# Kernel optimization log

Measured on AMD Instinct MI355X. Metric: run time of the kernel, lower is better.

Reference implementation:

```python
import jax, jax.numpy as jnp
import numpy as np

N = 50000      # nodes
E = 800000     # edges (avg degree 16)
D_IN = 16      # raw node feature dim
D = 64         # d_model
H = 8          # heads
DH = D // H    # dim_head = 8
L = 2          # num_encoder_layers
EPS = 1e-5
SCALE = float(np.sqrt(DH))


def _xavier(key, shape):
    fan_in, fan_out = shape[-2], shape[-1]
    a = float(np.sqrt(6.0 / (fan_in + fan_out)))
    return jax.random.uniform(key, shape, jnp.float32, -a, a)


def setup_inputs() -> dict:
    key = jax.random.key(0)
    ks = jax.random.split(key, 20)
    feat = jax.random.normal(ks[0], (N, D_IN), jnp.float32)
    src = jax.random.randint(ks[1], (E,), 0, N, jnp.int32)
    dst = jax.random.randint(ks[2], (E,), 0, N, jnp.int32)
    return {
        "feat": feat,
        "src": src,
        "dst": dst,
        "W_emb": _xavier(ks[3], (D_IN, D)),
        "b_emb": jnp.zeros((D,), jnp.float32),
        "Wq": _xavier(ks[4], (L, D, D)),
        "Wk": _xavier(ks[5], (L, D, D)),
        "Wv": _xavier(ks[6], (L, D, D)),
        "Wo": _xavier(ks[7], (L, D, D)),
        "bo": jnp.zeros((L, D), jnp.float32),
        "bn1_g": jnp.ones((L, D), jnp.float32),
        "bn1_b": jnp.zeros((L, D), jnp.float32),
        "W1": _xavier(ks[8], (L, D, 2 * D)),
        "b1": jnp.zeros((L, 2 * D), jnp.float32),
        "W2": _xavier(ks[9], (L, 2 * D, D)),
        "b2": jnp.zeros((L, D), jnp.float32),
        "bn2_g": jnp.ones((L, D), jnp.float32),
        "bn2_b": jnp.zeros((L, D), jnp.float32),
    }


def _batch_norm(x, g, b):
    # BatchNorm1d (training-mode forward: batch statistics, biased var)
    mu = jnp.mean(x, axis=0)
    var = jnp.var(x, axis=0)
    return (x - mu) / jnp.sqrt(var + EPS) * g + b


def _layer(h, src, dst, Wq, Wk, Wv, Wo, bo, bn1_g, bn1_b, W1, b1, W2, b2, bn2_g, bn2_b):
    h_in1 = h
    Q = (h @ Wq).reshape(N, H, DH)
    K = (h @ Wk).reshape(N, H, DH)
    V = (h @ Wv).reshape(N, H, DH)
    # SDDMM: per-edge dot(K[src], Q[dst]) -> [E, H]
    e = jnp.sum(K[src] * Q[dst], axis=-1)
    # scaled_exp: exp(clamp(score/sqrt(dh), -10, 10)) stored as edge 'score'
    e = jnp.exp(jnp.clip(e / SCALE, -10.0, 10.0))
    # reduce_func then applies a softmax over mailbox scores (double exp, faithful)
    m = jax.ops.segment_max(e, dst, num_segments=N)          # [N, H]
    w = jnp.exp(e - m[dst])                                   # [E, H]
    s = jax.ops.segment_sum(w, dst, num_segments=N)           # [N, H]
    alpha = w / s[dst]                                        # [E, H]
    out = jax.ops.segment_sum(alpha[:, :, None] * V[src], dst, num_segments=N)
    h = out.reshape(N, D) @ Wo + bo
    h = _batch_norm(h_in1 + h, bn1_g, bn1_b)
    h_in2 = h
    h = jax.nn.relu(h @ W1 + b1) @ W2 + b2
    h = _batch_norm(h + h_in2, bn2_g, bn2_b)
    return h


def reference(feat, src, dst, W_emb, b_emb, Wq, Wk, Wv, Wo, bo, bn1_g, bn1_b,
              W1, b1, W2, b2, bn2_g, bn2_b):
    h = feat @ W_emb + b_emb  # embedding_h (dropout=0)
    for l in range(L):
        h = _layer(h, src, dst, Wq[l], Wk[l], Wv[l], Wo[l], bo[l],
                   bn1_g[l], bn1_b[l], W1[l], b1[l], W2[l], b2[l],
                   bn2_g[l], bn2_b[l])
    return h
```

## Files before the change

kernel.cpp:

```cpp
#include <hip/hip_runtime.h>

#define NNODES 50000
#define NEDGES 800000
#define DM 64
#define NH 8
#define DH 8
#define EPSN 1e-5f
#define INV_SCALE 0.3535533905932738f
#define SCAN_BLOCKS 200
#define SCAN_CHUNK  250

template<int KA, int KB, int R, bool RELU, bool RES, bool STATS, bool BNRES>
__global__ __launch_bounds__(256, 4) void gemm_k(const float* __restrict__ A,
    const float* __restrict__ W, int woff,
    const float* __restrict__ bias, int boff,
    float* __restrict__ C, float* __restrict__ stats,
    const float* __restrict__ bnstats, const float* __restrict__ bng, int bgoff,
    const float* __restrict__ bnb, int bboff, int Nrows)
{
    constexpr int CG   = KB / 4;
    constexpr int RG   = 256 / CG;
    constexpr int ROWS = RG * R;
    constexpr int APAD = KA + 4;
    constexpr int KAq  = KA / 4;

    __shared__ __align__(16) float sW[KA * KB];
    __shared__ __align__(16) float sA[ROWS * APAD];

    const int tid  = threadIdx.x;
    const int row0 = blockIdx.x * ROWS;

    for (int i4 = tid; i4 < KA * KB / 4; i4 += 256)
        *(float4*)&sW[i4 * 4] = ((const float4*)(W + woff))[i4];
    for (int i4 = tid; i4 < ROWS * KAq; i4 += 256) {
        int r = i4 / KAq, kq = i4 - r * KAq;
        int gr = row0 + r;
        float4 v = make_float4(0.f, 0.f, 0.f, 0.f);
        if (gr < Nrows) v = ((const float4*)A)[(size_t)gr * KAq + kq];
        *(float4*)&sA[r * APAD + kq * 4] = v;
    }
    __syncthreads();

    const int cg = tid % CG, rg = tid / CG;
    const int c0 = cg * 4, r0 = rg * R;

    float4 acc[R];
#pragma unroll
    for (int rr = 0; rr < R; rr++) acc[rr] = make_float4(0.f, 0.f, 0.f, 0.f);

#pragma unroll 2
    for (int k = 0; k < KA; k += 4) {
        float4 w0 = *(const float4*)&sW[(k + 0) * KB + c0];
        float4 w1 = *(const float4*)&sW[(k + 1) * KB + c0];
        float4 w2 = *(const float4*)&sW[(k + 2) * KB + c0];
        float4 w3 = *(const float4*)&sW[(k + 3) * KB + c0];
#pragma unroll
        for (int rr = 0; rr < R; rr++) {
            float4 av = *(const float4*)&sA[(r0 + rr) * APAD + k];
            acc[rr].x += av.x * w0.x + av.y * w1.x + av.z * w2.x + av.w * w3.x;
            acc[rr].y += av.x * w0.y + av.y * w1.y + av.z * w2.y + av.w * w3.y;
            acc[rr].z += av.x * w0.z + av.y * w1.z + av.z * w2.z + av.w * w3.z;
            acc[rr].w += av.x * w0.w + av.y * w1.w + av.z * w2.w + av.w * w3.w;
        }
    }

    float4 bv = make_float4(0.f, 0.f, 0.f, 0.f);
    if (bias) {
        bv.x = bias[boff + c0];     bv.y = bias[boff + c0 + 1];
        bv.z = bias[boff + c0 + 2]; bv.w = bias[boff + c0 + 3];
    }

    float4 scR = make_float4(1.f, 1.f, 1.f, 1.f);
    float4 ofR = make_float4(0.f, 0.f, 0.f, 0.f);
    if (BNRES) {
        const float inv_n = 1.0f / NNODES;
#pragma unroll
        for (int j = 0; j < 4; j++) {
            float mu   = bnstats[c0 + j] * inv_n;
            float var  = bnstats[KB + c0 + j] * inv_n - mu * mu;
            float istd = rsqrtf(fmaxf(var, 0.f) + EPSN);
            float s    = istd * bng[bgoff + c0 + j];
            ((float*)&scR)[j] = s;
            ((float*)&ofR)[j] = bnb[bboff + c0 + j] - mu * s;
        }
    }

    float4 vals[R];
#pragma unroll
    for (int rr = 0; rr < R; rr++) {
        int grow = row0 + r0 + rr;
        bool valid = grow < Nrows;
        float4 v;
        v.x = acc[rr].x + bv.x; v.y = acc[rr].y + bv.y;
        v.z = acc[rr].z + bv.z; v.w = acc[rr].w + bv.w;
        if (RELU) {
            v.x = fmaxf(v.x, 0.f); v.y = fmaxf(v.y, 0.f);
            v.z = fmaxf(v.z, 0.f); v.w = fmaxf(v.w, 0.f);
        }
        if (valid) {
            if (RES) {
                float4 old = *(const float4*)&C[(size_t)grow * KB + c0];
                if (BNRES) {
                    old.x = old.x * scR.x + ofR.x;
                    old.y = old.y * scR.y + ofR.y;
                    old.z = old.z * scR.z + ofR.z;
                    old.w = old.w * scR.w + ofR.w;
                }
                v.x += old.x; v.y += old.y; v.z += old.z; v.w += old.w;
            }
            *(float4*)&C[(size_t)grow * KB + c0] = v;
        } else {
            v = make_float4(0.f, 0.f, 0.f, 0.f);
        }
        vals[rr] = v;
    }

    if (STATS) {
        __syncthreads();
        float4 cs = make_float4(0.f, 0.f, 0.f, 0.f);
#pragma unroll
        for (int rr = 0; rr < R; rr++) {
            cs.x += vals[rr].x; cs.y += vals[rr].y;
            cs.z += vals[rr].z; cs.w += vals[rr].w;
        }
        *(float4*)&sA[rg * KB + c0] = cs;
        __syncthreads();
        if (tid < KB) {
            float s = 0.f;
#pragma unroll
            for (int g = 0; g < RG; g++) s += sA[g * KB + tid];
            atomicAdd(&stats[tid], s);
        }
        __syncthreads();
        float4 cq = make_float4(0.f, 0.f, 0.f, 0.f);
#pragma unroll
        for (int rr = 0; rr < R; rr++) {
            cq.x += vals[rr].x * vals[rr].x; cq.y += vals[rr].y * vals[rr].y;
            cq.z += vals[rr].z * vals[rr].z; cq.w += vals[rr].w * vals[rr].w;
        }
        *(float4*)&sA[rg * KB + c0] = cq;
        __syncthreads();
        if (tid < KB) {
            float s = 0.f;
#pragma unroll
            for (int g = 0; g < RG; g++) s += sA[g * KB + tid];
            atomicAdd(&stats[KB + tid], s);
        }
    }
}

template<bool BNIN>
__global__ __launch_bounds__(256, 4) void qkv_k(const float* __restrict__ A,
    const float* __restrict__ Wq, const float* __restrict__ Wk,
    const float* __restrict__ Wv, int woff,
    float* __restrict__ Qo, float* __restrict__ Ko, float* __restrict__ Vo,
    const float* __restrict__ bnstats, const float* __restrict__ bng, int bgoff,
    const float* __restrict__ bnb, int bboff, int Nrows)
{
    constexpr int APAD = 68;
    __shared__ __align__(16) float sW[64 * 64];
    __shared__ __align__(16) float sA[64 * APAD];

    const int tid  = threadIdx.x;
    const int row0 = blockIdx.x * 64;

    {
        const int kq = tid & 15, cc = kq * 4;
        float4 sc = make_float4(1.f, 1.f, 1.f, 1.f);
        float4 of = make_float4(0.f, 0.f, 0.f, 0.f);
        if (BNIN) {
            const float inv_n = 1.0f / NNODES;
#pragma unroll
            for (int j = 0; j < 4; j++) {
                float mu   = bnstats[cc + j] * inv_n;
                float var  = bnstats[64 + cc + j] * inv_n - mu * mu;
                float istd = rsqrtf(fmaxf(var, 0.f) + EPSN);
                float s    = istd * bng[bgoff + cc + j];
                ((float*)&sc)[j] = s;
                ((float*)&of)[j] = bnb[bboff + cc + j] - mu * s;
            }
        }
        for (int i4 = tid; i4 < 64 * 16; i4 += 256) {
            int r = i4 >> 4;
            int gr = row0 + r;
            float4 v = make_float4(0.f, 0.f, 0.f, 0.f);
            if (gr < Nrows) {
                v = ((const float4*)A)[(size_t)gr * 16 + kq];
                if (BNIN) {
                    v.x = v.x * sc.x + of.x; v.y = v.y * sc.y + of.y;
                    v.z = v.z * sc.z + of.z; v.w = v.w * sc.w + of.w;
                }
            }
            *(float4*)&sA[r * APAD + cc] = v;
        }
    }

    const float* Ws[3]   = {Wq, Wk, Wv};
    float*       Outs[3] = {Qo, Ko, Vo};

    const int cg = tid & 15, rg = tid >> 4;
    const int c0 = cg * 4, r0 = rg * 4;

    for (int m = 0; m < 3; m++) {
        __syncthreads();
        for (int i4 = tid; i4 < 1024; i4 += 256)
            *(float4*)&sW[i4 * 4] = ((const float4*)(Ws[m] + woff))[i4];
        __syncthreads();

        float4 acc[4];
#pragma unroll
        for (int rr = 0; rr < 4; rr++) acc[rr] = make_float4(0.f, 0.f, 0.f, 0.f);

#pragma unroll 2
        for (int k = 0; k < 64; k += 4) {
            float4 w0 = *(const float4*)&sW[(k + 0) * 64 + c0];
            float4 w1 = *(const float4*)&sW[(k + 1) * 64 + c0];
            float4 w2 = *(const float4*)&sW[(k + 2) * 64 + c0];
            float4 w3 = *(const float4*)&sW[(k + 3) * 64 + c0];
#pragma unroll
            for (int rr = 0; rr < 4; rr++) {
                float4 av = *(const float4*)&sA[(r0 + rr) * APAD + k];
                acc[rr].x += av.x * w0.x + av.y * w1.x + av.z * w2.x + av.w * w3.x;
                acc[rr].y += av.x * w0.y + av.y * w1.y + av.z * w2.y + av.w * w3.y;
                acc[rr].z += av.x * w0.z + av.y * w1.z + av.z * w2.z + av.w * w3.z;
                acc[rr].w += av.x * w0.w + av.y * w1.w + av.z * w2.w + av.w * w3.w;
            }
        }

#pragma unroll
        for (int rr = 0; rr < 4; rr++) {
            int grow = row0 + r0 + rr;
            if (grow < Nrows)
                *(float4*)&Outs[m][(size_t)grow * 64 + c0] = acc[rr];
        }
    }
}

__global__ __launch_bounds__(256, 2) void ffn_k(float* __restrict__ H,
    const float* __restrict__ W1, int w1off,
    const float* __restrict__ b1, int b1off,
    const float* __restrict__ W2, int w2off,
    const float* __restrict__ b2, int b2off,
    const float* __restrict__ bnstats,
    const float* __restrict__ bng, int bgoff,
    const float* __restrict__ bnb, int bboff,
    float* __restrict__ stats2, int Nrows)
{
    constexpr int APAD = 68, FPAD = 132;
    __shared__ __align__(16) float sW[128 * 64];
    __shared__ __align__(16) float sA[32 * APAD];
    __shared__ __align__(16) float sF[32 * FPAD];

    const int tid  = threadIdx.x;
    const int row0 = blockIdx.x * 32;

    for (int i4 = tid; i4 < 2048; i4 += 256)
        *(float4*)&sW[i4 * 4] = ((const float4*)(W1 + w1off))[i4];

    {
        const int kq = tid & 15, cc = kq * 4;
        const float inv_n = 1.0f / NNODES;
        float4 sc, of;
#pragma unroll
        for (int j = 0; j < 4; j++) {
            float mu   = bnstats[cc + j] * inv_n;
            float var  = bnstats[64 + cc + j] * inv_n - mu * mu;
            float istd = rsqrtf(fmaxf(var, 0.f) + EPSN);
            float s    = istd * bng[bgoff + cc + j];
            ((float*)&sc)[j] = s;
            ((float*)&of)[j] = bnb[bboff + cc + j] - mu * s;
        }
        for (int i4 = tid; i4 < 512; i4 += 256) {
            int r = i4 >> 4;
            int gr = row0 + r;
            float4 v = make_float4(0.f, 0.f, 0.f, 0.f);
            if (gr < Nrows) {
                v = ((const float4*)H)[(size_t)gr * 16 + kq];
                v.x = v.x * sc.x + of.x; v.y = v.y * sc.y + of.y;
                v.z = v.z * sc.z + of.z; v.w = v.w * sc.w + of.w;
            }
            *(float4*)&sA[r * APAD + cc] = v;
        }
    }
    __syncthreads();

    {
        const int cg = tid & 31, rg = tid >> 5;
        const int c0 = cg * 4, r0 = rg * 4;
        float4 acc[4];
#pragma unroll
        for (int rr = 0; rr < 4; rr++) acc[rr] = make_float4(0.f, 0.f, 0.f, 0.f);
#pragma unroll 2
        for (int k = 0; k < 64; k += 4) {
            float4 w0 = *(const float4*)&sW[(k + 0) * 128 + c0];
            float4 w1 = *(const float4*)&sW[(k + 1) * 128 + c0];
            float4 w2 = *(const float4*)&sW[(k + 2) * 128 + c0];
            float4 w3 = *(const float4*)&sW[(k + 3) * 128 + c0];
#pragma unroll
            for (int rr = 0; rr < 4; rr++) {
                float4 av = *(const float4*)&sA[(r0 + rr) * APAD + k];
                acc[rr].x += av.x * w0.x + av.y * w1.x + av.z * w2.x + av.w * w3.x;
                acc[rr].y += av.x * w0.y + av.y * w1.y + av.z * w2.y + av.w * w3.y;
                acc[rr].z += av.x * w0.z + av.y * w1.z + av.z * w2.z + av.w * w3.z;
                acc[rr].w += av.x * w0.w + av.y * w1.w + av.z * w2.w + av.w * w3.w;
            }
        }
        float4 bb;
        bb.x = b1[b1off + c0];     bb.y = b1[b1off + c0 + 1];
        bb.z = b1[b1off + c0 + 2]; bb.w = b1[b1off + c0 + 3];
#pragma unroll
        for (int rr = 0; rr < 4; rr++) {
            float4 v;
            v.x = fmaxf(acc[rr].x + bb.x, 0.f);
            v.y = fmaxf(acc[rr].y + bb.y, 0.f);
            v.z = fmaxf(acc[rr].z + bb.z, 0.f);
            v.w = fmaxf(acc[rr].w + bb.w, 0.f);
            *(float4*)&sF[(r0 + rr) * FPAD + c0] = v;
        }
    }
    __syncthreads();

    for (int i4 = tid; i4 < 2048; i4 += 256)
        *(float4*)&sW[i4 * 4] = ((const float4*)(W2 + w2off))[i4];
    __syncthreads();

    const int cg = tid & 15, rg = tid >> 4;
    const int c0 = cg * 4, r0 = rg * 2;
    float4 acc[2];
#pragma unroll
    for (int rr = 0; rr < 2; rr++) acc[rr] = make_float4(0.f, 0.f, 0.f, 0.f);
#pragma unroll 2
    for (int k = 0; k < 128; k += 4) {
        float4 w0 = *(const float4*)&sW[(k + 0) * 64 + c0];
        float4 w1 = *(const float4*)&sW[(k + 1) * 64 + c0];
        float4 w2 = *(const float4*)&sW[(k + 2) * 64 + c0];
        float4 w3 = *(const float4*)&sW[(k + 3) * 64 + c0];
#pragma unroll
        for (int rr = 0; rr < 2; rr++) {
            float4 fv = *(const float4*)&sF[(r0 + rr) * FPAD + k];
            acc[rr].x += fv.x * w0.x + fv.y * w1.x + fv.z * w2.x + fv.w * w3.x;
            acc[rr].y += fv.x * w0.y + fv.y * w1.y + fv.z * w2.y + fv.w * w3.y;
            acc[rr].z += fv.x * w0.z + fv.y * w1.z + fv.z * w2.z + fv.w * w3.z;
            acc[rr].w += fv.x * w0.w + fv.y * w1.w + fv.z * w2.w + fv.w * w3.w;
        }
    }
    float4 bb;
    bb.x = b2[b2off + c0];     bb.y = b2[b2off + c0 + 1];
    bb.z = b2[b2off + c0 + 2]; bb.w = b2[b2off + c0 + 3];

    float4 vals[2];
#pragma unroll
    for (int rr = 0; rr < 2; rr++) {
        int grow = row0 + r0 + rr;
        bool valid = grow < Nrows;
        float4 res = *(const float4*)&sA[(r0 + rr) * APAD + c0];
        float4 v;
        v.x = acc[rr].x + bb.x + res.x;
        v.y = acc[rr].y + bb.y + res.y;
        v.z = acc[rr].z + bb.z + res.z;
        v.w = acc[rr].w + bb.w + res.w;
        if (valid) {
            *(float4*)&H[(size_t)grow * 64 + c0] = v;
        } else {
            v = make_float4(0.f, 0.f, 0.f, 0.f);
        }
        vals[rr] = v;
    }

    __syncthreads();
    float4 cs;
    cs.x = vals[0].x + vals[1].x; cs.y = vals[0].y + vals[1].y;
    cs.z = vals[0].z + vals[1].z; cs.w = vals[0].w + vals[1].w;
    *(float4*)&sA[rg * 64 + c0] = cs;
    __syncthreads();
    if (tid < 64) {
        float s = 0.f;
#pragma unroll
        for (int g = 0; g < 16; g++) s += sA[g * 64 + tid];
        atomicAdd(&stats2[tid], s);
    }
    __syncthreads();
    float4 cq;
    cq.x = vals[0].x * vals[0].x + vals[1].x * vals[1].x;
    cq.y = vals[0].y * vals[0].y + vals[1].y * vals[1].y;
    cq.z = vals[0].z * vals[0].z + vals[1].z * vals[1].z;
    cq.w = vals[0].w * vals[0].w + vals[1].w * vals[1].w;
    *(float4*)&sA[rg * 64 + c0] = cq;
    __syncthreads();
    if (tid < 64) {
        float s = 0.f;
#pragma unroll
        for (int g = 0; g < 16; g++) s += sA[g * 64 + tid];
        atomicAdd(&stats2[64 + tid], s);
    }
}

__global__ __launch_bounds__(256) void bn_apply(const float* __restrict__ Hin,
    float* __restrict__ Hout, const float* __restrict__ stats,
    const float* __restrict__ g, int goff, const float* __restrict__ b, int boff)
{
    int i = blockIdx.x * 256 + threadIdx.x;
    if (i >= NNODES * DM) return;
    int c = i & 63;
    float mu  = stats[c] * (1.0f / NNODES);
    float var = stats[64 + c] * (1.0f / NNODES) - mu * mu;
    float istd = rsqrtf(fmaxf(var, 0.0f) + EPSN);
    Hout[i] = (Hin[i] - mu) * istd * g[goff + c] + b[boff + c];
}

__global__ __launch_bounds__(256) void zero_int_k(int* __restrict__ p, int n)
{
    int i = blockIdx.x * 256 + threadIdx.x;
    if (i < n) p[i] = 0;
}

__global__ __launch_bounds__(256) void count_k(const int* __restrict__ dst,
                                               int* __restrict__ cursor)
{
    int e = blockIdx.x * 256 + threadIdx.x;
    if (e < NEDGES) atomicAdd(&cursor[dst[e]], 1);
}

__global__ __launch_bounds__(256) void csr_scanA(const int* __restrict__ cursor,
                                                 int* __restrict__ bsum)
{
    __shared__ int red[256];
    const int base = blockIdx.x * SCAN_CHUNK;
    int s = 0;
    for (int i = threadIdx.x; i < SCAN_CHUNK; i += 256) s += cursor[base + i];
    red[threadIdx.x] = s;
    __syncthreads();
    for (int o = 128; o > 0; o >>= 1) {
        if (threadIdx.x < o) red[threadIdx.x] += red[threadIdx.x + o];
        __syncthreads();
    }
    if (threadIdx.x == 0) bsum[blockIdx.x] = red[0];
}

__global__ __launch_bounds__(256) void csr_scanB(int* __restrict__ bsum)
{
    __shared__ int t[256];
    const int tid = threadIdx.x;
    int v = (tid < SCAN_BLOCKS) ? bsum[tid] : 0;
    t[tid] = v;
    __syncthreads();
    for (int off = 1; off < 256; off <<= 1) {
        int x = (tid >= off) ? t[tid - off] : 0;
        __syncthreads();
        t[tid] += x;
        __syncthreads();
    }
    if (tid < SCAN_BLOCKS) bsum[tid] = t[tid] - v;
}

__global__ __launch_bounds__(256) void csr_scanC(int* __restrict__ cursor,
    int* __restrict__ rowptr, const int* __restrict__ bsum)
{
    __shared__ int t[256];
    const int base = blockIdx.x * SCAN_CHUNK;
    const int tid  = threadIdx.x;
    int deg = (tid < SCAN_CHUNK) ? cursor[base + tid] : 0;
    t[tid] = deg;
    __syncthreads();
    for (int off = 1; off < 256; off <<= 1) {
        int x = (tid >= off) ? t[tid - off] : 0;
        __syncthreads();
        t[tid] += x;
        __syncthreads();
    }
    int excl = bsum[blockIdx.x] + t[tid] - deg;
    if (tid < SCAN_CHUNK) {
        rowptr[base + tid] = excl;
        cursor[base + tid] = excl;
    }
    if (blockIdx.x == 0 && tid == 0) rowptr[NNODES] = NEDGES;
}

__global__ __launch_bounds__(256) void fill_k(const int* __restrict__ src,
    const int* __restrict__ dst, int* __restrict__ cursor,
    int* __restrict__ nbr)
{
    int e = blockIdx.x * 256 + threadIdx.x;
    if (e >= NEDGES) return;
    int pos = atomicAdd(&cursor[dst[e]], 1);
    nbr[pos] = src[e];
}

__global__ __launch_bounds__(256) void attn_fused_k(const float* __restrict__ Q,
    const float* __restrict__ K, const float* __restrict__ V,
    const int* __restrict__ rowptr, const int* __restrict__ nbr,
    float* __restrict__ U)
{
    const int w = threadIdx.x >> 6;
    const int d = blockIdx.x * 4 + w;
    if (d >= NNODES) return;
    const int l  = threadIdx.x & 63;
    const int el = l >> 3;
    const int h  = l & 7;
    const int e0 = rowptr[d], e1 = rowptr[d + 1];
    const int deg = e1 - e0;

    if (deg == 0) {
        U[(size_t)d * DM + h * DH + el] = 0.f;
        return;
    }

    const float4* qp = (const float4*)(Q + (size_t)d * DM + h * DH);
    const float4 q0 = qp[0], q1 = qp[1];

    float m = 0.0f;
    float S = 0.0f;
    float u[8] = {0.f, 0.f, 0.f, 0.f, 0.f, 0.f, 0.f, 0.f};

    for (int base = 0; base < deg; base += 16) {
        const int i0 = base + el, i1 = base + 8 + el;
        const bool v0ok = i0 < deg, v1ok = i1 < deg;
        const int s0 = nbr[e0 + (v0ok ? i0 : 0)];
        const int s1 = nbr[e0 + (v1ok ? i1 : 0)];

        const float4* kp0 = (const float4*)(K + (size_t)s0 * DM + h * DH);
        const float4* vp0 = (const float4*)(V + (size_t)s0 * DM + h * DH);
        const float4* kp1 = (const float4*)(K + (size_t)s1 * DM + h * DH);
        const float4* vp1 = (const float4*)(V + (size_t)s1 * DM + h * DH);
        float4 ka0 = kp0[0], ka1 = kp0[1];
        float4 kb0 = kp1[0], kb1 = kp1[1];
        float4 va0 = vp0[0], va1 = vp0[1];
        float4 vb0 = vp1[0], vb1 = vp1[1];

        float d0 = ka0.x * q0.x + ka0.y * q0.y + ka0.z * q0.z + ka0.w * q0.w
                 + ka1.x * q1.x + ka1.y * q1.y + ka1.z * q1.z + ka1.w * q1.w;
        float d1 = kb0.x * q0.x + kb0.y * q0.y + kb0.z * q0.z + kb0.w * q0.w
                 + kb1.x * q1.x + kb1.y * q1.y + kb1.z * q1.z + kb1.w * q1.w;

        float ev0 = __expf(fminf(fmaxf(d0 * INV_SCALE, -10.f), 10.f));
        float ev1 = __expf(fminf(fmaxf(d1 * INV_SCALE, -10.f), 10.f));
        if (!v0ok) ev0 = 0.f;
        if (!v1ok) ev1 = 0.f;

        float bm = fmaxf(ev0, ev1);
        bm = fmaxf(bm, __shfl_xor(bm, 8, 64));
        bm = fmaxf(bm, __shfl_xor(bm, 16, 64));
        bm = fmaxf(bm, __shfl_xor(bm, 32, 64));

        const float mn = fmaxf(m, bm);
        const float r  = __expf(m - mn);
        const float w0 = v0ok ? __expf(ev0 - mn) : 0.f;
        const float w1 = v1ok ? __expf(ev1 - mn) : 0.f;

        S = S * r + w0 + w1;
        u[0] = u[0] * r + w0 * va0.x + w1 * vb0.x;
        u[1] = u[1] * r + w0 * va0.y + w1 * vb0.y;
        u[2] = u[2] * r + w0 * va0.z + w1 * vb0.z;
        u[3] = u[3] * r + w0 * va0.w + w1 * vb0.w;
        u[4] = u[4] * r + w0 * va1.x + w1 * vb1.x;
        u[5] = u[5] * r + w0 * va1.y + w1 * vb1.y;
        u[6] = u[6] * r + w0 * va1.z + w1 * vb1.z;
        u[7] = u[7] * r + w0 * va1.w + w1 * vb1.w;
        m = mn;
    }

#pragma unroll
    for (int off = 8; off <= 32; off <<= 1) {
        S += __shfl_xor(S, off, 64);
#pragma unroll
        for (int j = 0; j < 8; j++) u[j] += __shfl_xor(u[j], off, 64);
    }

    const float out = (S > 0.f) ? u[el] / S : 0.f;
    U[(size_t)d * DM + h * DH + el] = out;
}

__global__ __launch_bounds__(256) void fill_const_k(float* __restrict__ out, int n)
{
    int i = blockIdx.x * 256 + threadIdx.x;
    if (i < n) out[i] = 100.0f;
}

extern "C" void kernel_launch(void* const* d_in, const int* in_sizes, int n_in,
                              void* d_out, int out_size, void* d_ws, size_t ws_size,
                              hipStream_t stream)
{
    const int expect[18] = {800000, 800000, 800000, 1024, 64,
                            8192, 8192, 8192, 8192, 128,
                            128, 128, 16384, 256, 16384, 128, 128, 128};
    bool order_ok = (n_in == 18) && (out_size == NNODES * DM);
    if (order_ok)
        for (int i = 0; i < 18; i++)
            if (in_sizes[i] != expect[i]) { order_ok = false; break; }
    if (!order_ok) {
        fill_const_k<<<(out_size + 255) / 256, 256, 0, stream>>>((float*)d_out,
                                                                 out_size);
        return;
    }

    const float* feat  = (const float*)d_in[0];
    const int*   src   = (const int*)d_in[1];
    const int*   dst   = (const int*)d_in[2];
    const float* W_emb = (const float*)d_in[3];
    const float* b_emb = (const float*)d_in[4];
    const float* Wq    = (const float*)d_in[5];
    const float* Wk    = (const float*)d_in[6];
    const float* Wv    = (const float*)d_in[7];
    const float* Wo    = (const float*)d_in[8];
    const float* bo    = (const float*)d_in[9];
    const float* bn1_g = (const float*)d_in[10];
    const float* bn1_b = (const float*)d_in[11];
    const float* W1    = (const float*)d_in[12];
    const float* b1    = (const float*)d_in[13];
    const float* W2    = (const float*)d_in[14];
    const float* b2    = (const float*)d_in[15];
    const float* bn2_g = (const float*)d_in[16];
    const float* bn2_b = (const float*)d_in[17];

    const size_t ND = (size_t)NNODES * DM;
    float* ws     = (float*)d_ws;
    float* Hb     = ws;
    float* Qb     = Hb + ND;
    float* Kb     = Qb + ND;
    float* Vb     = Kb + ND;
    float* Ub     = Vb + ND;
    float* stats  = Ub + ND;
    int*   rowptr = (int*)(stats + 256);
    int*   cursor = rowptr + (NNODES + 1);
    int*   bsum   = cursor + NNODES;
    int*   nbr    = bsum + SCAN_BLOCKS;

    float* statsA = stats;
    float* statsB = stats + 128;

    const size_t BASE = (5 * ND + 256) * 4
                      + ((NNODES + 1) + NNODES + SCAN_BLOCKS + NEDGES) * 4;
    if (ws_size < BASE) {
        fill_const_k<<<(out_size + 255) / 256, 256, 0, stream>>>((float*)d_out,
                                                                 out_size);
        return;
    }

    const int g64 = (NNODES + 63) / 64;
    const int g32 = (NNODES + 31) / 32;
    const int gND = (int)(ND / 256);
    const int gE  = (NEDGES + 255) / 256;
    const int gAT = (NNODES + 3) / 4;

    zero_int_k<<<(NNODES + 255) / 256, 256, 0, stream>>>(cursor, NNODES);
    count_k<<<gE, 256, 0, stream>>>(dst, cursor);
    csr_scanA<<<SCAN_BLOCKS, 256, 0, stream>>>(cursor, bsum);
    csr_scanB<<<1, 256, 0, stream>>>(bsum);
    csr_scanC<<<SCAN_BLOCKS, 256, 0, stream>>>(cursor, rowptr, bsum);
    fill_k<<<gE, 256, 0, stream>>>(src, dst, cursor, nbr);

    gemm_k<16, 64, 4, false, false, false, false>
        <<<g64, 256, 0, stream>>>(feat, W_emb, 0, b_emb, 0, Hb, nullptr,
                                  nullptr, nullptr, 0, nullptr, 0, NNODES);

    for (int l = 0; l < 2; l++) {
        const int woff  = l * DM * DM;
        const int w1off = l * DM * 2 * DM;
        const int boff  = l * DM;
        const int b1off = l * 2 * DM;
        const int poff  = (l - 1) * DM;

        if (l == 0)
            qkv_k<false><<<g64, 256, 0, stream>>>(Hb, Wq, Wk, Wv, woff,
                Qb, Kb, Vb, nullptr, nullptr, 0, nullptr, 0, NNODES);
        else
            qkv_k<true><<<g64, 256, 0, stream>>>(Hb, Wq, Wk, Wv, woff,
                Qb, Kb, Vb, statsB, bn2_g, poff, bn2_b, poff, NNODES);

        attn_fused_k<<<gAT, 256, 0, stream>>>(Qb, Kb, Vb, rowptr, nbr, Ub);

        hipMemsetAsync(statsA, 0, 128 * 4, stream);
        if (l == 0)
            gemm_k<64, 64, 4, false, true, true, false>
                <<<g64, 256, 0, stream>>>(Ub, Wo, woff, bo, boff, Hb, statsA,
                                          nullptr, nullptr, 0, nullptr, 0, NNODES);
        else
            gemm_k<64, 64, 4, false, true, true, true>
                <<<g64, 256, 0, stream>>>(Ub, Wo, woff, bo, boff, Hb, statsA,
                                          statsB, bn2_g, poff, bn2_b, poff, NNODES);

        hipMemsetAsync(statsB, 0, 128 * 4, stream);
        ffn_k<<<g32, 256, 0, stream>>>(Hb, W1, w1off, b1, b1off,
                                       W2, w1off, b2, boff,
                                       statsA, bn1_g, boff, bn1_b, boff,
                                       statsB, NNODES);
    }

    bn_apply<<<gND, 256, 0, stream>>>(Hb, (float*)d_out, statsB,
                                      bn2_g, DM, bn2_b, DM);
}
```

Baseline: 545.6 us.

## Fuse attention aggregation with output projection, residual and BN stats

Merges the edge-softmax aggregation kernel with the Wo projection GEMM, including the residual add, the optional previous BatchNorm apply and the per-column statistics accumulation. Each block loads Wo into shared memory, and each wave handles four destination nodes sequentially. It multiplies each node's aggregated row by Wo from shared memory before writing H. This removes the U intermediate buffer round trip and one kernel launch, but cuts the number of blocks by four and serialises four nodes per wave. That may reduce latency hiding for the irregular gathers and adds a 16KB shared-memory footprint per block.

```diff
diff --git a/kernel.cpp b/kernel.cpp
--- a/kernel.cpp
+++ b/kernel.cpp
@@ -486,88 +486,147 @@
     nbr[pos] = src[e];
 }
 
-__global__ __launch_bounds__(256) void attn_fused_k(const float* __restrict__ Q,
+template<bool BNRES>
+__global__ __launch_bounds__(256) void attn_wo_k(const float* __restrict__ Q,
     const float* __restrict__ K, const float* __restrict__ V,
     const int* __restrict__ rowptr, const int* __restrict__ nbr,
-    float* __restrict__ U)
-{
-    const int w = threadIdx.x >> 6;
-    const int d = blockIdx.x * 4 + w;
-    if (d >= NNODES) return;
-    const int l  = threadIdx.x & 63;
-    const int el = l >> 3;
-    const int h  = l & 7;
-    const int e0 = rowptr[d], e1 = rowptr[d + 1];
-    const int deg = e1 - e0;
-
-    if (deg == 0) {
-        U[(size_t)d * DM + h * DH + el] = 0.f;
-        return;
-    }
-
-    const float4* qp = (const float4*)(Q + (size_t)d * DM + h * DH);
-    const float4 q0 = qp[0], q1 = qp[1];
-
-    float m = 0.0f;
-    float S = 0.0f;
-    float u[8] = {0.f, 0.f, 0.f, 0.f, 0.f, 0.f, 0.f, 0.f};
-
-    for (int base = 0; base < deg; base += 16) {
-        const int i0 = base + el, i1 = base + 8 + el;
-        const bool v0ok = i0 < deg, v1ok = i1 < deg;
-        const int s0 = nbr[e0 + (v0ok ? i0 : 0)];
-        const int s1 = nbr[e0 + (v1ok ? i1 : 0)];
-
-        const float4* kp0 = (const float4*)(K + (size_t)s0 * DM + h * DH);
-        const float4* vp0 = (const float4*)(V + (size_t)s0 * DM + h * DH);
-        const float4* kp1 = (const float4*)(K + (size_t)s1 * DM + h * DH);
-        const float4* vp1 = (const float4*)(V + (size_t)s1 * DM + h * DH);
-        float4 ka0 = kp0[0], ka1 = kp0[1];
-        float4 kb0 = kp1[0], kb1 = kp1[1];
-        float4 va0 = vp0[0], va1 = vp0[1];
-        float4 vb0 = vp1[0], vb1 = vp1[1];
-
-        float d0 = ka0.x * q0.x + ka0.y * q0.y + ka0.z * q0.z + ka0.w * q0.w
-                 + ka1.x * q1.x + ka1.y * q1.y + ka1.z * q1.z + ka1.w * q1.w;
-        float d1 = kb0.x * q0.x + kb0.y * q0.y + kb0.z * q0.z + kb0.w * q0.w
-                 + kb1.x * q1.x + kb1.y * q1.y + kb1.z * q1.z + kb1.w * q1.w;
-
-        float ev0 = __expf(fminf(fmaxf(d0 * INV_SCALE, -10.f), 10.f));
-        float ev1 = __expf(fminf(fmaxf(d1 * INV_SCALE, -10.f), 10.f));
-        if (!v0ok) ev0 = 0.f;
-        if (!v1ok) ev1 = 0.f;
-
-        float bm = fmaxf(ev0, ev1);
-        bm = fmaxf(bm, __shfl_xor(bm, 8, 64));
-        bm = fmaxf(bm, __shfl_xor(bm, 16, 64));
-        bm = fmaxf(bm, __shfl_xor(bm, 32, 64));
-
-        const float mn = fmaxf(m, bm);
-        const float r  = __expf(m - mn);
-        const float w0 = v0ok ? __expf(ev0 - mn) : 0.f;
-        const float w1 = v1ok ? __expf(ev1 - mn) : 0.f;
-
-        S = S * r + w0 + w1;
-        u[0] = u[0] * r + w0 * va0.x + w1 * vb0.x;
-        u[1] = u[1] * r + w0 * va0.y + w1 * vb0.y;
-        u[2] = u[2] * r + w0 * va0.z + w1 * vb0.z;
-        u[3] = u[3] * r + w0 * va0.w + w1 * vb0.w;
-        u[4] = u[4] * r + w0 * va1.x + w1 * vb1.x;
-        u[5] = u[5] * r + w0 * va1.y + w1 * vb1.y;
-        u[6] = u[6] * r + w0 * va1.z + w1 * vb1.z;
-        u[7] = u[7] * r + w0 * va1.w + w1 * vb1.w;
-        m = mn;
-    }
-
-#pragma unroll
-    for (int off = 8; off <= 32; off <<= 1) {
-        S += __shfl_xor(S, off, 64);
-#pragma unroll
-        for (int j = 0; j < 8; j++) u[j] += __shfl_xor(u[j], off, 64);
-    }
-
-    const float out = (S > 0.f) ? u[el] / S : 0.f;
-    U[(size_t)d * DM + h * DH + el] = out;
+    const float* __restrict__ Wo, int woff,
+    const float* __restrict__ bo, int boff,
+    float* __restrict__ H, float* __restrict__ statsA,
+    const float* __restrict__ bnstats,
+    const float* __restrict__ bng, int bgoff,
+    const float* __restrict__ bnb, int bboff)
+{
+    __shared__ __align__(16) float sWo[64 * 64];
+    __shared__ __align__(16) float sU[4][64];
+    __shared__ __align__(16) float sR[4 * 64];
+
+    const int tid = threadIdx.x;
+    const int w   = tid >> 6;
+    const int l   = tid & 63;
+    const int el  = l >> 3;
+    const int h   = l & 7;
+
+    for (int i4 = tid; i4 < 1024; i4 += 256)
+        *(float4*)&sWo[i4 * 4] = ((const float4*)(Wo + woff))[i4];
+    __syncthreads();
+
+    float scp = 1.f, ofp = 0.f;
+    if (BNRES) {
+        const float inv_n = 1.0f / NNODES;
+        float mu   = bnstats[l] * inv_n;
+        float var  = bnstats[64 + l] * inv_n - mu * mu;
+        float istd = rsqrtf(fmaxf(var, 0.f) + EPSN);
+        scp = istd * bng[bgoff + l];
+        ofp = bnb[bboff + l] - mu * scp;
+    }
+    const float boc = bo[boff + l];
+
+    float csum = 0.f, cqsum = 0.f;
+    const int d0 = blockIdx.x * 16 + w * 4;
+
+    for (int t = 0; t < 4; t++) {
+        const int d = d0 + t;
+        const int e0 = rowptr[d], e1 = rowptr[d + 1];
+        const int deg = e1 - e0;
+
+        float outv = 0.f;
+        if (deg > 0) {
+            const float4* qp = (const float4*)(Q + (size_t)d * DM + h * DH);
+            const float4 q0 = qp[0], q1 = qp[1];
+
+            float m = 0.0f, S = 0.0f;
+            float u[8] = {0.f, 0.f, 0.f, 0.f, 0.f, 0.f, 0.f, 0.f};
+
+            for (int base = 0; base < deg; base += 16) {
+                const int i0 = base + el, i1 = base + 8 + el;
+                const bool v0ok = i0 < deg, v1ok = i1 < deg;
+                const int s0 = nbr[e0 + (v0ok ? i0 : 0)];
+                const int s1 = nbr[e0 + (v1ok ? i1 : 0)];
+
+                const float4* kp0 = (const float4*)(K + (size_t)s0 * DM + h * DH);
+                const float4* vp0 = (const float4*)(V + (size_t)s0 * DM + h * DH);
+                const float4* kp1 = (const float4*)(K + (size_t)s1 * DM + h * DH);
+                const float4* vp1 = (const float4*)(V + (size_t)s1 * DM + h * DH);
+                float4 ka0 = kp0[0], ka1 = kp0[1];
+                float4 kb0 = kp1[0], kb1 = kp1[1];
+                float4 va0 = vp0[0], va1 = vp0[1];
+                float4 vb0 = vp1[0], vb1 = vp1[1];
+
+                float dd0 = ka0.x * q0.x + ka0.y * q0.y + ka0.z * q0.z + ka0.w * q0.w
+                          + ka1.x * q1.x + ka1.y * q1.y + ka1.z * q1.z + ka1.w * q1.w;
+                float dd1 = kb0.x * q0.x + kb0.y * q0.y + kb0.z * q0.z + kb0.w * q0.w
+                          + kb1.x * q1.x + kb1.y * q1.y + kb1.z * q1.z + kb1.w * q1.w;
+
+                float ev0 = __expf(fminf(fmaxf(dd0 * INV_SCALE, -10.f), 10.f));
+                float ev1 = __expf(fminf(fmaxf(dd1 * INV_SCALE, -10.f), 10.f));
+                if (!v0ok) ev0 = 0.f;
+                if (!v1ok) ev1 = 0.f;
+
+                float bm = fmaxf(ev0, ev1);
+                bm = fmaxf(bm, __shfl_xor(bm, 8, 64));
+                bm = fmaxf(bm, __shfl_xor(bm, 16, 64));
+                bm = fmaxf(bm, __shfl_xor(bm, 32, 64));
+
+                const float mn = fmaxf(m, bm);
+                const float r  = __expf(m - mn);
+                const float w0 = v0ok ? __expf(ev0 - mn) : 0.f;
+                const float w1 = v1ok ? __expf(ev1 - mn) : 0.f;
+
+                S = S * r + w0 + w1;
+                u[0] = u[0] * r + w0 * va0.x + w1 * vb0.x;
+                u[1] = u[1] * r + w0 * va0.y + w1 * vb0.y;
+                u[2] = u[2] * r + w0 * va0.z + w1 * vb0.z;
+                u[3] = u[3] * r + w0 * va0.w + w1 * vb0.w;
+                u[4] = u[4] * r + w0 * va1.x + w1 * vb1.x;
+                u[5] = u[5] * r + w0 * va1.y + w1 * vb1.y;
+                u[6] = u[6] * r + w0 * va1.z + w1 * vb1.z;
+                u[7] = u[7] * r + w0 * va1.w + w1 * vb1.w;
+                m = mn;
+            }
+
+#pragma unroll
+            for (int off = 8; off <= 32; off <<= 1) {
+                S += __shfl_xor(S, off, 64);
+#pragma unroll
+                for (int j = 0; j < 8; j++) u[j] += __shfl_xor(u[j], off, 64);
+            }
+            outv = (S > 0.f) ? u[el] / S : 0.f;
+        }
+
+        sU[w][h * 8 + el] = outv;
+
+        float acc = 0.f;
+#pragma unroll
+        for (int k4 = 0; k4 < 16; k4++) {
+            float4 uu = *(const float4*)&sU[w][k4 * 4];
+            acc += uu.x * sWo[(k4 * 4 + 0) * 64 + l];
+            acc += uu.y * sWo[(k4 * 4 + 1) * 64 + l];
+            acc += uu.z * sWo[(k4 * 4 + 2) * 64 + l];
+            acc += uu.w * sWo[(k4 * 4 + 3) * 64 + l];
+        }
+
+        float res = H[(size_t)d * DM + l];
+        if (BNRES) res = res * scp + ofp;
+        float v = acc + boc + res;
+        H[(size_t)d * DM + l] = v;
+        csum  += v;
+        cqsum += v * v;
+    }
+
+    sR[w * 64 + l] = csum;
+    __syncthreads();
+    if (tid < 64) {
+        float s = sR[tid] + sR[64 + tid] + sR[128 + tid] + sR[192 + tid];
+        atomicAdd(&statsA[tid], s);
+    }
+    __syncthreads();
+    sR[w * 64 + l] = cqsum;
+    __syncthreads();
+    if (tid < 64) {
+        float s = sR[tid] + sR[64 + tid] + sR[128 + tid] + sR[192 + tid];
+        atomicAdd(&statsA[64 + tid], s);
+    }
 }
 
 __global__ __launch_bounds__(256) void fill_const_k(float* __restrict__ out, int n)
@@ -640,7 +699,7 @@
     const int g32 = (NNODES + 31) / 32;
     const int gND = (int)(ND / 256);
     const int gE  = (NEDGES + 255) / 256;
-    const int gAT = (NNODES + 3) / 4;
+    const int gAW = NNODES / 16;
 
     zero_int_k<<<(NNODES + 255) / 256, 256, 0, stream>>>(cursor, NNODES);
     count_k<<<gE, 256, 0, stream>>>(dst, cursor);
@@ -667,17 +726,15 @@
             qkv_k<true><<<g64, 256, 0, stream>>>(Hb, Wq, Wk, Wv, woff,
                 Qb, Kb, Vb, statsB, bn2_g, poff, bn2_b, poff, NNODES);
 
-        attn_fused_k<<<gAT, 256, 0, stream>>>(Qb, Kb, Vb, rowptr, nbr, Ub);
-
         hipMemsetAsync(statsA, 0, 128 * 4, stream);
         if (l == 0)
-            gemm_k<64, 64, 4, false, true, true, false>
-                <<<g64, 256, 0, stream>>>(Ub, Wo, woff, bo, boff, Hb, statsA,
-                                          nullptr, nullptr, 0, nullptr, 0, NNODES);
+            attn_wo_k<false><<<gAW, 256, 0, stream>>>(Qb, Kb, Vb, rowptr, nbr,
+                Wo, woff, bo, boff, Hb, statsA,
+                nullptr, nullptr, 0, nullptr, 0);
         else
-            gemm_k<64, 64, 4, false, true, true, true>
-                <<<g64, 256, 0, stream>>>(Ub, Wo, woff, bo, boff, Hb, statsA,
-                                          statsB, bn2_g, poff, bn2_b, poff, NNODES);
+            attn_wo_k<true><<<gAW, 256, 0, stream>>>(Qb, Kb, Vb, rowptr, nbr,
+                Wo, woff, bo, boff, Hb, statsA,
+                statsB, bn2_g, poff, bn2_b, poff);
 
         hipMemsetAsync(statsB, 0, 128 * 4, stream);
         ffn_k<<<g32, 256, 0, stream>>>(Hb, W1, w1off, b1, b1off,
```

Measured after the change: 604.9 us. 10.9% more time.
